# Optimization experiments

Measured on AMD Instinct MI355X. Metric: run time of the kernel, lower is better.

Reference implementation:

```python
import jax, jax.numpy as jnp
import numpy as np

N = 50000       # num vertices
E_SEG = 80000   # num hyperedges
NNZ = 400000    # incidence pairs
FIN = 512       # input feature dim
H = 256         # MLP_hidden
C = 40          # num classes
NLAYER = 2      # All_num_layers
ALPHA = 0.5     # restart_alpha


def _w(k, shape):
    return jax.random.normal(k, shape, jnp.float32) * (1.0 / np.sqrt(shape[0]))


def setup_inputs() -> dict:
    key = jax.random.key(0)
    ks = jax.random.split(key, 12)
    return {
        "x": jax.random.normal(ks[0], (N, FIN), jnp.float32),
        "vertex": jax.random.randint(ks[1], (NNZ,), 0, N),
        "edges": jax.random.randint(ks[2], (NNZ,), 0, E_SEG),
        "lin_in_w": _w(ks[3], (FIN, H)), "lin_in_b": jnp.zeros((H,), jnp.float32),
        "w1": _w(ks[4], (H, H)),   "b1": jnp.zeros((H,), jnp.float32),
        "w2": _w(ks[5], (2 * H, H)), "b2": jnp.zeros((H,), jnp.float32),
        "w3": _w(ks[6], (H, H)),   "b3": jnp.zeros((H,), jnp.float32),
        "cls_w1": _w(ks[7], (H, H)), "cls_b1": jnp.zeros((H,), jnp.float32),
        "cls_w2": _w(ks[8], (H, C)), "cls_b2": jnp.zeros((C,), jnp.float32),
    }


def reference(x, vertex, edges, lin_in_w, lin_in_b, w1, b1, w2, b2, w3, b3,
              cls_w1, cls_b1, cls_w2, cls_b2):
    # input projection (dropout is identity at p=0)
    x = jax.nn.relu(x @ lin_in_w + lin_in_b)           # [N, H]
    x0 = x
    for _ in range(NLAYER):  # same conv weights reused each layer
        # W1 (1-layer MLP = Linear), gather to incidences
        xve = (x @ w1 + b1)[vertex]                    # [NNZ, H]
        # scatter-add to hyperedges
        xe = jax.ops.segment_sum(xve, edges, num_segments=E_SEG)  # [E, H]
        # gather back, concat with vertex feats, W2 (Linear on 2H)
        xev = jnp.concatenate([x[vertex], xe[edges]], axis=-1) @ w2 + b2  # [NNZ, H]
        # scatter-add to vertices
        xv = jax.ops.segment_sum(xev, vertex, num_segments=N)     # [N, H]
        # restart connection + W (Linear) + outer activation
        x = (1.0 - ALPHA) * xv + ALPHA * x0
        x = jax.nn.relu(x @ w3 + b3)
    # classifier MLP (2 layers: Linear -> relu -> Linear)
    h = jax.nn.relu(x @ cls_w1 + cls_b1)
    return h @ cls_w2 + cls_b2                          # [N, C]
```

## Files before the change

### kernel.cpp

```cpp
#include <hip/hip_runtime.h>
#include <hip/hip_bf16.h>
#include <cstdint>
#include <cstddef>

#define HD   256
#define NV   50000
#define NE   80000
#define NNZC 400000
#define FINC 512
#define NCLS 40

using bf16 = __hip_bfloat16;

typedef short bf16x8v __attribute__((ext_vector_type(8)));
typedef float f32x4   __attribute__((ext_vector_type(4)));

#define NCH_E ((NE + 1023) / 1024)
#define NCH_V ((NV + 1023) / 1024)

__device__ __forceinline__ float b2f(unsigned short u) {
    union { unsigned int i; float f; } c; c.i = ((unsigned int)u) << 16; return c.f;
}
__device__ __forceinline__ unsigned short f2b(float f) {
    union { float f; unsigned int i; } c; c.f = f;
    return (unsigned short)((c.i + 0x7FFFu + ((c.i >> 16) & 1u)) >> 16);
}
__device__ __forceinline__ float4 load4f(const bf16* p) {
    ushort4 u = *reinterpret_cast<const ushort4*>(p);
    return make_float4(b2f(u.x), b2f(u.y), b2f(u.z), b2f(u.w));
}
__device__ __forceinline__ void store4(bf16* p, float4 v) {
    ushort4 u; u.x = f2b(v.x); u.y = f2b(v.y); u.z = f2b(v.z); u.w = f2b(v.w);
    *reinterpret_cast<ushort4*>(p) = u;
}

__device__ __forceinline__ void gl_lds16(const bf16* g, short* l) {
    __builtin_amdgcn_global_load_lds(
        (const __attribute__((address_space(1))) unsigned int*)g,
        (__attribute__((address_space(3))) unsigned int*)l,
        16, 0, 0);
}

__global__ __launch_bounds__(256)
void fill0_k(unsigned int* __restrict__ p, long long n)
{
    long long i = (long long)blockIdx.x * 256 + threadIdx.x;
    long long stride = (long long)gridDim.x * 256;
    for (; i < n; i += stride) p[i] = 0u;
}

__global__ __launch_bounds__(256)
void hist_k(const int* __restrict__ vertex, const int* __restrict__ edges,
            int* __restrict__ cnt_v, int* __restrict__ cnt_e, int nnz)
{
    int i = blockIdx.x * 256 + threadIdx.x;
    if (i < nnz) {
        atomicAdd(&cnt_v[vertex[i]], 1);
        atomicAdd(&cnt_e[edges[i]], 1);
    }
}

__global__ __launch_bounds__(256)
void scan_part2_k(const int* __restrict__ cnt_e, int* __restrict__ off_e, int* __restrict__ part_e,
                  const int* __restrict__ cnt_v, int* __restrict__ off_v, int* __restrict__ part_v)
{
    const int* cnt; int* off; int* part; int n;
    if (blockIdx.y == 0) { cnt = cnt_e; off = off_e; part = part_e; n = NE; }
    else                 { cnt = cnt_v; off = off_v; part = part_v; n = NV; }
    int base = blockIdx.x * 1024;
    if (base >= n) return;
    __shared__ int s[256];
    int idx = base + threadIdx.x * 4;
    int v[4], sum = 0;
    #pragma unroll
    for (int j = 0; j < 4; ++j) { v[j] = (idx + j < n) ? cnt[idx + j] : 0; sum += v[j]; }
    s[threadIdx.x] = sum;
    __syncthreads();
    #pragma unroll
    for (int d = 1; d < 256; d <<= 1) {
        int t = (threadIdx.x >= d) ? s[threadIdx.x - d] : 0;
        __syncthreads();
        s[threadIdx.x] += t;
        __syncthreads();
    }
    int excl = s[threadIdx.x] - sum;
    #pragma unroll
    for (int j = 0; j < 4; ++j) {
        if (idx + j < n) off[idx + j] = excl;
        excl += v[j];
    }
    if (threadIdx.x == 255) part[blockIdx.x] = s[255];
}

__global__ __launch_bounds__(256)
void scan_top2_k(int* __restrict__ part_e, int* __restrict__ end_e,
                 int* __restrict__ part_v, int* __restrict__ end_v)
{
    int* part; int* endp; int nch;
    if (blockIdx.x == 0) { part = part_e; endp = end_e; nch = NCH_E; }
    else                 { part = part_v; endp = end_v; nch = NCH_V; }
    __shared__ int s[256];
    int v = (threadIdx.x < nch) ? part[threadIdx.x] : 0;
    s[threadIdx.x] = v;
    __syncthreads();
    #pragma unroll
    for (int d = 1; d < 256; d <<= 1) {
        int t = (threadIdx.x >= d) ? s[threadIdx.x - d] : 0;
        __syncthreads();
        s[threadIdx.x] += t;
        __syncthreads();
    }
    if (threadIdx.x < nch) part[threadIdx.x] = s[threadIdx.x] - v;
    if (threadIdx.x == 255) *endp = s[255];
}

__global__ __launch_bounds__(256)
void scan_addcur2_k(int* __restrict__ off_e, const int* __restrict__ part_e, int* __restrict__ cur_e,
                    int* __restrict__ off_v, const int* __restrict__ part_v, int* __restrict__ cur_v)
{
    int n; int* off; const int* part; int* cur;
    if (blockIdx.y == 0) { n = NE; off = off_e; part = part_e; cur = cur_e; }
    else                 { n = NV; off = off_v; part = part_v; cur = cur_v; }
    int i = blockIdx.x * 256 + threadIdx.x;
    if (i < n) { int o = off[i] + part[i >> 10]; off[i] = o; cur[i] = o; }
}

__global__ __launch_bounds__(256)
void csr_fill_k(const int* __restrict__ vertex, const int* __restrict__ edges,
                int* __restrict__ cur_e, int* __restrict__ cur_v,
                int* __restrict__ adj_e, int* __restrict__ adj_v, int nnz)
{
    int i = blockIdx.x * 256 + threadIdx.x;
    if (i >= nnz) return;
    int v = vertex[i], e = edges[i];
    adj_e[atomicAdd(&cur_e[e], 1)] = v;
    adj_v[atomicAdd(&cur_v[v], 1)] = e;
}

__global__ __launch_bounds__(256)
void prep_w_k(const float* __restrict__ lin_w, const float* __restrict__ w1,
              const float* __restrict__ w2, const float* __restrict__ w3,
              const float* __restrict__ cw1, const float* __restrict__ cw2,
              const float* __restrict__ b2,
              unsigned short* __restrict__ lin_wt, unsigned short* __restrict__ w1t,
              unsigned short* __restrict__ w2a_nb, unsigned short* __restrict__ w2b_nb,
              unsigned short* __restrict__ w3t, unsigned short* __restrict__ cw1t,
              unsigned short* __restrict__ cw2t, float* __restrict__ b2w3)
{
    int idx = blockIdx.x * 256 + threadIdx.x;
    if (idx < 131072) { int n = idx >> 9, k = idx & 511; lin_wt[idx] = f2b(lin_w[k * 256 + n]); return; }
    idx -= 131072;
    if (idx < 65536) { int n = idx >> 8, k = idx & 255; w1t[idx] = f2b(w1[k * 256 + n]); return; }
    idx -= 65536;
    if (idx < 65536) { w2a_nb[idx] = f2b(w2[idx]); return; }
    idx -= 65536;
    if (idx < 65536) { w2b_nb[idx] = f2b(w2[65536 + idx]); return; }
    idx -= 65536;
    if (idx < 65536) { int n = idx >> 8, k = idx & 255; w3t[idx] = f2b(w3[k * 256 + n]); return; }
    idx -= 65536;
    if (idx < 65536) { int n = idx >> 8, k = idx & 255; cw1t[idx] = f2b(cw1[k * 256 + n]); return; }
    idx -= 65536;
    if (idx < 12288) { int n = idx >> 8, k = idx & 255; cw2t[idx] = f2b((n < NCLS) ? cw2[k * NCLS + n] : 0.f); return; }
    idx -= 12288;
    if (idx < 256) {
        float s = 0.f;
        for (int k = 0; k < 256; ++k) s += b2[k] * w3[k * 256 + idx];
        b2w3[idx] = s;
    }
}

template<int EPI, bool AF32>
__global__ __launch_bounds__(256)
void mgemm_k(const void* __restrict__ Agv, const bf16* __restrict__ Bt,
             const float* __restrict__ bias, const float* __restrict__ bias2,
             const int* __restrict__ deg,
             const bf16* __restrict__ Sb, const bf16* __restrict__ z0b,
             const float* __restrict__ b2w3v,
             bf16* __restrict__ Cg, bf16* __restrict__ Cg2, bf16* __restrict__ Cg3,
             int M, int K, int Nc)
{
    const int nbn = Nc >> 7;
    const int nbm = (M + 127) >> 7;
    const int p   = blockIdx.x;
    const int xcd = p & 7;
    const int q   = p >> 3;
    const int cblk = q % nbn;
    const int rblk = q / nbn;
    const int rb   = rblk * 8 + xcd;
    if (rb >= nbm) return;
    const int bn = cblk * 128;
    const int bm = rb * 128;

    __shared__ __align__(16) short As[128 * 64];
    __shared__ __align__(16) short Bs[128 * 64];

    const int t  = threadIdx.x;
    const int wv = t >> 6, l = t & 63;
    const int wr = wv >> 1, wc = wv & 1;
    const int l15 = l & 15;

    f32x4 acc[4][4];
    #pragma unroll
    for (int m = 0; m < 4; ++m)
        #pragma unroll
        for (int n = 0; n < 4; ++n)
            acc[m][n] = (f32x4){0.f, 0.f, 0.f, 0.f};

    const int brow8   = l >> 3;
    const int bcol_sw = (((l & 7) ^ (l >> 3)) * 8);

    for (int k0 = 0; k0 < K; k0 += 64) {
        if constexpr (AF32) {
            const float* Af = (const float*)Agv;
            #pragma unroll
            for (int pi = 0; pi < 4; ++pi) {
                int idx8 = pi * 256 + t;
                int row  = idx8 >> 3;
                int cg   = (idx8 & 7) * 8;
                int ga = bm + row; if (ga >= M) ga = M - 1;
                const float* src = Af + (size_t)ga * K + k0 + cg;
                f32x4 u = *reinterpret_cast<const f32x4*>(src);
                f32x4 v = *reinterpret_cast<const f32x4*>(src + 4);
                bf16x8v o;
                o[0] = (short)f2b(u[0]); o[1] = (short)f2b(u[1]);
                o[2] = (short)f2b(u[2]); o[3] = (short)f2b(u[3]);
                o[4] = (short)f2b(v[0]); o[5] = (short)f2b(v[1]);
                o[6] = (short)f2b(v[2]); o[7] = (short)f2b(v[3]);
                *reinterpret_cast<bf16x8v*>(As + row * 64 + (cg ^ ((row & 7) * 8))) = o;
            }
        } else {
            const bf16* Ab = (const bf16*)Agv;
            #pragma unroll
            for (int i = 0; i < 4; ++i) {
                int c = wv * 4 + i;
                int row = c * 8 + brow8;
                int ga = bm + row; if (ga >= M) ga = M - 1;
                gl_lds16(Ab + (size_t)ga * K + k0 + bcol_sw, As + c * 512);
            }
        }
        #pragma unroll
        for (int i = 0; i < 4; ++i) {
            int c = wv * 4 + i;
            int row = c * 8 + brow8;
            gl_lds16(Bt + (size_t)(bn + row) * K + k0 + bcol_sw, Bs + c * 512);
        }
        __syncthreads();

        #pragma unroll
        for (int ks = 0; ks < 2; ++ks) {
            bf16x8v a[4], b[4];
            const int kb = ks * 64 + (l >> 4) * 16;
            #pragma unroll
            for (int m = 0; m < 4; ++m) {
                int r = wr * 64 + m * 16 + l15;
                a[m] = *reinterpret_cast<const bf16x8v*>(
                           (const char*)As + r * 128 + (kb ^ ((r & 7) << 4)));
            }
            #pragma unroll
            for (int n = 0; n < 4; ++n) {
                int r = wc * 64 + n * 16 + l15;
                b[n] = *reinterpret_cast<const bf16x8v*>(
                           (const char*)Bs + r * 128 + (kb ^ ((r & 7) << 4)));
            }
            #pragma unroll
            for (int m = 0; m < 4; ++m)
                #pragma unroll
                for (int n = 0; n < 4; ++n)
                    acc[m][n] = __builtin_amdgcn_mfma_f32_16x16x32_bf16(a[m], b[n], acc[m][n], 0, 0, 0);
        }
        __syncthreads();
    }

    if (EPI == 3) {
        int oi = bn >> 8;
        bf16* CC = (oi == 0) ? Cg : (oi == 1) ? Cg2 : Cg3;
        const float* bb = (oi == 0) ? bias : (oi == 1) ? bias2 : nullptr;
        int cb = bn & 255;
        float bv[4];
        #pragma unroll
        for (int n = 0; n < 4; ++n)
            bv[n] = bb ? bb[cb + wc * 64 + n * 16 + l15] : 0.f;
        #pragma unroll
        for (int m = 0; m < 4; ++m) {
            #pragma unroll
            for (int i = 0; i < 4; ++i) {
                int row = bm + wr * 64 + m * 16 + (l >> 4) * 4 + i;
                if (row >= M) continue;
                size_t base = (size_t)row * 256 + cb + wc * 64 + l15;
                #pragma unroll
                for (int n = 0; n < 4; ++n)
                    reinterpret_cast<unsigned short*>(CC)[base + n * 16] = f2b(acc[m][n][i] + bv[n]);
            }
        }
    } else if (EPI == 4) {
        float bv[4], bw[4];
        #pragma unroll
        for (int n = 0; n < 4; ++n) {
            int col = bn + wc * 64 + n * 16 + l15;
            bv[n] = bias[col];
            bw[n] = b2w3v[col];
        }
        #pragma unroll
        for (int m = 0; m < 4; ++m) {
            #pragma unroll
            for (int i = 0; i < 4; ++i) {
                int row = bm + wr * 64 + m * 16 + (l >> 4) * 4 + i;
                if (row >= M) continue;
                float d = (float)deg[row];
                size_t base = (size_t)row * Nc + bn + wc * 64 + l15;
                #pragma unroll
                for (int n = 0; n < 4; ++n) {
                    size_t idx = base + (size_t)n * 16;
                    float sv = b2f(reinterpret_cast<const unsigned short*>(Sb)[idx]);
                    float zv = b2f(reinterpret_cast<const unsigned short*>(z0b)[idx]);
                    float v = 0.5f * (d * (sv + bw[n]) + acc[m][n][i]) + 0.5f * zv + bv[n];
                    v = fmaxf(v, 0.f);
                    reinterpret_cast<unsigned short*>(Cg)[idx] = f2b(v);
                }
            }
        }
    } else {
        float bv[4];
        #pragma unroll
        for (int n = 0; n < 4; ++n)
            bv[n] = bias ? bias[bn + wc * 64 + n * 16 + l15] : 0.f;
        #pragma unroll
        for (int m = 0; m < 4; ++m) {
            #pragma unroll
            for (int i = 0; i < 4; ++i) {
                int row = bm + wr * 64 + m * 16 + (l >> 4) * 4 + i;
                if (row >= M) continue;
                size_t base = (size_t)row * Nc + bn + wc * 64 + l15;
                #pragma unroll
                for (int n = 0; n < 4; ++n) {
                    float v = acc[m][n][i] + bv[n];
                    if (EPI == 1) v = fmaxf(v, 0.f);
                    reinterpret_cast<unsigned short*>(Cg)[base + n * 16] = f2b(v);
                }
            }
        }
    }
}

__global__ __launch_bounds__(256)
void gather_sum_k(const bf16* __restrict__ src, const int* __restrict__ adj,
                  const int* __restrict__ off, bf16* __restrict__ dst, int nseg)
{
    int seg = blockIdx.x * 4 + (threadIdx.x >> 6);
    if (seg >= nseg) return;
    int lane = threadIdx.x & 63;
    int s0 = off[seg], s1 = off[seg + 1];
    float4 acc = make_float4(0.f, 0.f, 0.f, 0.f);
    int j = s0;
    for (; j + 4 <= s1; j += 4) {
        int r0 = adj[j], r1 = adj[j + 1], r2 = adj[j + 2], r3 = adj[j + 3];
        float4 v0 = load4f(src + (size_t)r0 * HD + lane * 4);
        float4 v1 = load4f(src + (size_t)r1 * HD + lane * 4);
        float4 v2 = load4f(src + (size_t)r2 * HD + lane * 4);
        float4 v3 = load4f(src + (size_t)r3 * HD + lane * 4);
        acc.x += (v0.x + v1.x) + (v2.x + v3.x);
        acc.y += (v0.y + v1.y) + (v2.y + v3.y);
        acc.z += (v0.z + v1.z) + (v2.z + v3.z);
        acc.w += (v0.w + v1.w) + (v2.w + v3.w);
    }
    for (; j < s1; ++j) {
        float4 v = load4f(src + (size_t)adj[j] * HD + lane * 4);
        acc.x += v.x; acc.y += v.y; acc.z += v.z; acc.w += v.w;
    }
    store4(dst + (size_t)seg * HD + lane * 4, acc);
}

__global__ __launch_bounds__(256)
void cls_mfma_k(const bf16* __restrict__ Hm, const bf16* __restrict__ Wt,
                const float* __restrict__ bias, float* __restrict__ out, int M)
{
    const int wv = threadIdx.x >> 6, l = threadIdx.x & 63;
    const int l15 = l & 15;
    const int r0 = blockIdx.x * 64 + wv * 16;
    f32x4 acc[3];
    #pragma unroll
    for (int n = 0; n < 3; ++n) acc[n] = (f32x4){0.f, 0.f, 0.f, 0.f};

    int arow = r0 + l15; if (arow >= M) arow = M - 1;
    const int ko = (l >> 4) * 8;
    for (int kk = 0; kk < HD; kk += 32) {
        bf16x8v a = *reinterpret_cast<const bf16x8v*>(Hm + (size_t)arow * HD + kk + ko);
        #pragma unroll
        for (int n = 0; n < 3; ++n) {
            bf16x8v b = *reinterpret_cast<const bf16x8v*>(Wt + (size_t)(n * 16 + l15) * HD + kk + ko);
            acc[n] = __builtin_amdgcn_mfma_f32_16x16x32_bf16(a, b, acc[n], 0, 0, 0);
        }
    }
    #pragma unroll
    for (int n = 0; n < 3; ++n) {
        int col = n * 16 + l15;
        if (col >= NCLS) continue;
        float bv = bias[col];
        #pragma unroll
        for (int i = 0; i < 4; ++i) {
            int row = r0 + (l >> 4) * 4 + i;
            if (row < M) out[(size_t)row * NCLS + col] = acc[n][i] + bv;
        }
    }
}

static inline int xcd_grid(int M, int Nc)
{
    int nbm = (M + 127) >> 7;
    int nbn = Nc >> 7;
    return nbn * (((nbm + 7) / 8) * 8);
}

extern "C" void kernel_launch(void* const* d_in, const int* in_sizes, int n_in,
                              void* d_out, int out_size, void* d_ws, size_t ws_size,
                              hipStream_t stream)
{
    const float* x_in   = (const float*)d_in[0];
    const int*   vertex = (const int*)d_in[1];
    const int*   edges  = (const int*)d_in[2];
    const float* lin_w  = (const float*)d_in[3];
    const float* lin_b  = (const float*)d_in[4];
    const float* w1     = (const float*)d_in[5];
    const float* b1     = (const float*)d_in[6];
    const float* w2     = (const float*)d_in[7];
    const float* b2     = (const float*)d_in[8];
    const float* w3     = (const float*)d_in[9];
    const float* b3     = (const float*)d_in[10];
    const float* cw1    = (const float*)d_in[11];
    const float* cb1    = (const float*)d_in[12];
    const float* cw2    = (const float*)d_in[13];
    const float* cb2    = (const float*)d_in[14];
    float* out = (float*)d_out;
    (void)in_sizes; (void)n_in; (void)out_size; (void)ws_size;

    char* ws = (char*)d_ws;
    const size_t nvhd = (size_t)NV * HD, nehd = (size_t)NE * HD;
    size_t off = 0;
    auto alloc = [&](size_t bytes) { char* p = ws + off; off += (bytes + 255) & ~(size_t)255; return p; };
    bf16* x0 = (bf16*)alloc(nvhd * 2);
    bf16* xA = (bf16*)alloc(nvhd * 2);
    bf16* E1 = (bf16*)alloc(nehd * 2);
    bf16* E2 = (bf16*)alloc(nehd * 2);
    bf16* S  = (bf16*)alloc(nvhd * 2);
    bf16* z0 = (bf16*)alloc(nvhd * 2);
    unsigned short* w1t    = (unsigned short*)alloc(3 * 256 * 256 * 2);
    unsigned short* W23at  = w1t + 65536;
    unsigned short* w3t    = w1t + 131072;
    unsigned short* W23bt  = (unsigned short*)alloc(256 * 256 * 2);
    unsigned short* w2ab   = (unsigned short*)alloc(512 * 256 * 2);
    unsigned short* w2a_nb = w2ab;
    unsigned short* w2b_nb = w2ab + 256 * 256;
    unsigned short* lin_wt = (unsigned short*)alloc(256 * 512 * 2);
    unsigned short* cw1t   = (unsigned short*)alloc(256 * 256 * 2);
    unsigned short* cw2t   = (unsigned short*)alloc(48 * 256 * 2);
    float* b2w3 = (float*)alloc(256 * 4);
    int* cnt_e = (int*)alloc(NE * 4);
    int* cnt_v = (int*)alloc(NV * 4);
    int* off_e = (int*)alloc((NE + 1) * 4);
    int* off_v = (int*)alloc((NV + 1) * 4);
    int* cur_e = (int*)alloc(NE * 4);
    int* cur_v = (int*)alloc(NV * 4);
    int* part_e = (int*)alloc(256 * 4);
    int* part_v = (int*)alloc(256 * 4);
    int* adj_e = (int*)alloc((size_t)NNZC * 4);
    int* adj_v = (int*)alloc((size_t)NNZC * 4);

    dim3 blk(256);

    fill0_k<<<128, blk, 0, stream>>>((unsigned int*)cnt_e, NE + NV);
    hist_k<<<(NNZC + 255) / 256, blk, 0, stream>>>(vertex, edges, cnt_v, cnt_e, NNZC);
    scan_part2_k<<<dim3(NCH_E, 2), blk, 0, stream>>>(cnt_e, off_e, part_e, cnt_v, off_v, part_v);
    scan_top2_k<<<2, blk, 0, stream>>>(part_e, off_e + NE, part_v, off_v + NV);
    scan_addcur2_k<<<dim3((NE + 255) / 256, 2), blk, 0, stream>>>(off_e, part_e, cur_e,
                                                                  off_v, part_v, cur_v);
    csr_fill_k<<<(NNZC + 255) / 256, blk, 0, stream>>>(vertex, edges, cur_e, cur_v, adj_e, adj_v, NNZC);

    prep_w_k<<<1841, blk, 0, stream>>>(lin_w, w1, w2, w3, cw1, cw2, b2,
                                       lin_wt, w1t, w2a_nb, w2b_nb, w3t, cw1t, cw2t, b2w3);
    mgemm_k<3, false><<<xcd_grid(256, 512), blk, 0, stream>>>((const bf16*)w3t, (const bf16*)w2ab,
        nullptr, nullptr, nullptr, nullptr, nullptr, nullptr,
        (bf16*)W23at, (bf16*)W23bt, nullptr, 256, 256, 512);

    mgemm_k<1, true><<<xcd_grid(NV, 256), blk, 0, stream>>>(x_in, (const bf16*)lin_wt,
        lin_b, nullptr, nullptr, nullptr, nullptr, nullptr,
        x0, nullptr, nullptr, NV, FINC, HD);

    const bf16* cur = x0;
    for (int layer = 0; layer < 2; ++layer) {
        if (layer == 0) {
            mgemm_k<3, false><<<xcd_grid(NV, 768), blk, 0, stream>>>(cur, (const bf16*)w1t,
                b1, nullptr, nullptr, nullptr, nullptr, nullptr,
                E1, S, z0, NV, HD, 768);
        } else {
            mgemm_k<3, false><<<xcd_grid(NV, 512), blk, 0, stream>>>(cur, (const bf16*)w1t,
                b1, nullptr, nullptr, nullptr, nullptr, nullptr,
                E1, S, nullptr, NV, HD, 512);
        }
        gather_sum_k<<<(NE + 3) / 4, blk, 0, stream>>>(E1, adj_e, off_e, E2, NE);
        gather_sum_k<<<(NV + 3) / 4, blk, 0, stream>>>(E2, adj_v, off_v, E1, NV);
        mgemm_k<4, false><<<xcd_grid(NV, 256), blk, 0, stream>>>(E1, (const bf16*)W23bt,
            b3, nullptr, cnt_v, S, z0, b2w3,
            xA, nullptr, nullptr, NV, HD, HD);
        cur = xA;
    }

    mgemm_k<1, false><<<xcd_grid(NV, 256), blk, 0, stream>>>(xA, (const bf16*)cw1t,
        cb1, nullptr, nullptr, nullptr, nullptr, nullptr,
        E1, nullptr, nullptr, NV, HD, HD);
    cls_mfma_k<<<(NV + 63) / 64, blk, 0, stream>>>(E1, (const bf16*)cw2t, cb2, out, NV);
}
```

Baseline: 470.8 us.

## Fuse vertex gather-sum into the W23 GEMM epilogue kernel

```diff
diff --git a/kernel.cpp b/kernel.cpp
--- a/kernel.cpp
+++ b/kernel.cpp
@@ -337,6 +337,134 @@
                     if (EPI == 1) v = fmaxf(v, 0.f);
                     reinterpret_cast<unsigned short*>(Cg)[base + n * 16] = f2b(v);
                 }
+            }
+        }
+    }
+}
+
+__global__ __launch_bounds__(256)
+void epi4g_k(const bf16* __restrict__ xe, const int* __restrict__ adj,
+             const int* __restrict__ off, const bf16* __restrict__ Bt,
+             const float* __restrict__ b3v, const float* __restrict__ b2w3v,
+             const int* __restrict__ deg,
+             const bf16* __restrict__ Sb, const bf16* __restrict__ z0b,
+             bf16* __restrict__ Cg, int M)
+{
+    __shared__ __align__(16) short As[64 * 256];
+    __shared__ __align__(16) short Bs[256 * 64];
+
+    const int t  = threadIdx.x;
+    const int wv = t >> 6, l = t & 63;
+    const int l15 = l & 15;
+    const int bm = blockIdx.x * 64;
+
+    const int brow8   = l >> 3;
+    const int bcol_sw = (((l & 7) ^ (l >> 3)) * 8);
+
+    #pragma unroll
+    for (int i = 0; i < 8; ++i) {
+        int c = wv * 8 + i;
+        int row = c * 8 + brow8;
+        gl_lds16(Bt + (size_t)row * 256 + bcol_sw, Bs + c * 512);
+    }
+
+    for (int rr = 0; rr < 16; ++rr) {
+        int r = wv * 16 + rr;
+        int v = bm + r;
+        float4 acc = make_float4(0.f, 0.f, 0.f, 0.f);
+        if (v < M) {
+            int s0 = off[v], s1 = off[v + 1];
+            int j = s0;
+            for (; j + 4 <= s1; j += 4) {
+                int r0 = adj[j], r1 = adj[j + 1], r2 = adj[j + 2], r3 = adj[j + 3];
+                float4 v0 = load4f(xe + (size_t)r0 * HD + l * 4);
+                float4 v1 = load4f(xe + (size_t)r1 * HD + l * 4);
+                float4 v2 = load4f(xe + (size_t)r2 * HD + l * 4);
+                float4 v3 = load4f(xe + (size_t)r3 * HD + l * 4);
+                acc.x += (v0.x + v1.x) + (v2.x + v3.x);
+                acc.y += (v0.y + v1.y) + (v2.y + v3.y);
+                acc.z += (v0.z + v1.z) + (v2.z + v3.z);
+                acc.w += (v0.w + v1.w) + (v2.w + v3.w);
+            }
+            for (; j < s1; ++j) {
+                float4 vv = load4f(xe + (size_t)adj[j] * HD + l * 4);
+                acc.x += vv.x; acc.y += vv.y; acc.z += vv.z; acc.w += vv.w;
+            }
+        }
+        short4 o;
+        o.x = (short)f2b(acc.x); o.y = (short)f2b(acc.y);
+        o.z = (short)f2b(acc.z); o.w = (short)f2b(acc.w);
+        int cb = l * 8;
+        *reinterpret_cast<short4*>((char*)As + r * 512 + (cb ^ ((r & 7) << 4))) = o;
+    }
+    __syncthreads();
+
+    f32x4 acc[4][4];
+    #pragma unroll
+    for (int m = 0; m < 4; ++m)
+        #pragma unroll
+        for (int n = 0; n < 4; ++n)
+            acc[m][n] = (f32x4){0.f, 0.f, 0.f, 0.f};
+
+    #pragma unroll
+    for (int k0 = 0; k0 < 4; ++k0) {
+        #pragma unroll
+        for (int ks = 0; ks < 2; ++ks) {
+            bf16x8v a[4], b[4];
+            const int kb = ks * 64 + (l >> 4) * 16;
+            #pragma unroll
+            for (int m = 0; m < 4; ++m) {
+                int r = m * 16 + l15;
+                a[m] = *reinterpret_cast<const bf16x8v*>(
+                           (const char*)As + r * 512 + ((k0 * 128 + kb) ^ ((r & 7) << 4)));
+            }
+            #pragma unroll
+            for (int n = 0; n < 4; ++n) {
+                int r = wv * 64 + n * 16 + l15;
+                b[n] = *reinterpret_cast<const bf16x8v*>(
+                           (const char*)Bs + r * 128 + (kb ^ ((r & 7) << 4)));
+            }
+            #pragma unroll
+            for (int m = 0; m < 4; ++m)
+                #pragma unroll
+                for (int n = 0; n < 4; ++n)
+                    acc[m][n] = __builtin_amdgcn_mfma_f32_16x16x32_bf16(a[m], b[n], acc[m][n], 0, 0, 0);
+        }
+        __syncthreads();
+        if (k0 < 3) {
+            #pragma unroll
+            for (int i = 0; i < 8; ++i) {
+                int c = wv * 8 + i;
+                int row = c * 8 + brow8;
+                gl_lds16(Bt + (size_t)row * 256 + (k0 + 1) * 64 + bcol_sw, Bs + c * 512);
+            }
+            __syncthreads();
+        }
+    }
+
+    float bv[4], bw[4];
+    #pragma unroll
+    for (int n = 0; n < 4; ++n) {
+        int col = wv * 64 + n * 16 + l15;
+        bv[n] = b3v[col];
+        bw[n] = b2w3v[col];
+    }
+    #pragma unroll
+    for (int m = 0; m < 4; ++m) {
+        #pragma unroll
+        for (int i = 0; i < 4; ++i) {
+            int row = bm + m * 16 + (l >> 4) * 4 + i;
+            if (row >= M) continue;
+            float d = (float)deg[row];
+            size_t base = (size_t)row * 256 + wv * 64 + l15;
+            #pragma unroll
+            for (int n = 0; n < 4; ++n) {
+                size_t idx = base + (size_t)n * 16;
+                float sv = b2f(reinterpret_cast<const unsigned short*>(Sb)[idx]);
+                float zv = b2f(reinterpret_cast<const unsigned short*>(z0b)[idx]);
+                float v = 0.5f * (d * (sv + bw[n]) + acc[m][n][i]) + 0.5f * zv + bv[n];
+                v = fmaxf(v, 0.f);
+                reinterpret_cast<unsigned short*>(Cg)[idx] = f2b(v);
             }
         }
     }
@@ -497,10 +625,8 @@
                 E1, S, nullptr, NV, HD, 512);
         }
         gather_sum_k<<<(NE + 3) / 4, blk, 0, stream>>>(E1, adj_e, off_e, E2, NE);
-        gather_sum_k<<<(NV + 3) / 4, blk, 0, stream>>>(E2, adj_v, off_v, E1, NV);
-        mgemm_k<4, false><<<xcd_grid(NV, 256), blk, 0, stream>>>(E1, (const bf16*)W23bt,
-            b3, nullptr, cnt_v, S, z0, b2w3,
-            xA, nullptr, nullptr, NV, HD, HD);
+        epi4g_k<<<(NV + 63) / 64, blk, 0, stream>>>(E2, adj_v, off_v, (const bf16*)W23bt,
+            b3, b2w3, cnt_v, S, z0, xA, NV);
         cur = xA;
     }
 
```

New measurement: 549.8 us. 1.17x slower.

## Fold W1 into the post-aggregation weight and gather raw vertex features

Applied to the files above, without the earlier changes.

```diff
diff --git a/kernel.cpp b/kernel.cpp
--- a/kernel.cpp
+++ b/kernel.cpp
@@ -138,11 +138,32 @@
 }
 
 __global__ __launch_bounds__(256)
+void dege2_k(const int* __restrict__ cnt_e, const int* __restrict__ adj_v,
+             const int* __restrict__ off_v, int* __restrict__ dege2, int n)
+{
+    int v = blockIdx.x * 256 + threadIdx.x;
+    if (v >= n) return;
+    int s = 0;
+    for (int j = off_v[v]; j < off_v[v + 1]; ++j) s += cnt_e[adj_v[j]];
+    dege2[v] = s;
+}
+
+__global__ __launch_bounds__(256)
+void b1w23_k(const float* __restrict__ b1, const unsigned short* __restrict__ W23bt,
+             float* __restrict__ o)
+{
+    int n = threadIdx.x;
+    float s = 0.f;
+    for (int k = 0; k < 256; ++k) s += b1[k] * b2f(W23bt[n * 256 + k]);
+    o[n] = s;
+}
+
+__global__ __launch_bounds__(256)
 void prep_w_k(const float* __restrict__ lin_w, const float* __restrict__ w1,
               const float* __restrict__ w2, const float* __restrict__ w3,
               const float* __restrict__ cw1, const float* __restrict__ cw2,
               const float* __restrict__ b2,
-              unsigned short* __restrict__ lin_wt, unsigned short* __restrict__ w1t,
+              unsigned short* __restrict__ lin_wt, unsigned short* __restrict__ w1_nb,
               unsigned short* __restrict__ w2a_nb, unsigned short* __restrict__ w2b_nb,
               unsigned short* __restrict__ w3t, unsigned short* __restrict__ cw1t,
               unsigned short* __restrict__ cw2t, float* __restrict__ b2w3)
@@ -150,7 +171,7 @@
     int idx = blockIdx.x * 256 + threadIdx.x;
     if (idx < 131072) { int n = idx >> 9, k = idx & 511; lin_wt[idx] = f2b(lin_w[k * 256 + n]); return; }
     idx -= 131072;
-    if (idx < 65536) { int n = idx >> 8, k = idx & 255; w1t[idx] = f2b(w1[k * 256 + n]); return; }
+    if (idx < 65536) { w1_nb[idx] = f2b(w1[idx]); return; }
     idx -= 65536;
     if (idx < 65536) { w2a_nb[idx] = f2b(w2[idx]); return; }
     idx -= 65536;
@@ -173,9 +194,9 @@
 __global__ __launch_bounds__(256)
 void mgemm_k(const void* __restrict__ Agv, const bf16* __restrict__ Bt,
              const float* __restrict__ bias, const float* __restrict__ bias2,
-             const int* __restrict__ deg,
+             const int* __restrict__ deg, const int* __restrict__ dege2,
              const bf16* __restrict__ Sb, const bf16* __restrict__ z0b,
-             const float* __restrict__ b2w3v,
+             const float* __restrict__ b2w3v, const float* __restrict__ b1w23v,
              bf16* __restrict__ Cg, bf16* __restrict__ Cg2, bf16* __restrict__ Cg3,
              int M, int K, int Nc)
 {
@@ -293,12 +314,13 @@
             }
         }
     } else if (EPI == 4) {
-        float bv[4], bw[4];
+        float bv[4], bw[4], bb1[4];
         #pragma unroll
         for (int n = 0; n < 4; ++n) {
             int col = bn + wc * 64 + n * 16 + l15;
-            bv[n] = bias[col];
-            bw[n] = b2w3v[col];
+            bv[n]  = bias[col];
+            bw[n]  = b2w3v[col];
+            bb1[n] = b1w23v[col];
         }
         #pragma unroll
         for (int m = 0; m < 4; ++m) {
@@ -306,14 +328,16 @@
             for (int i = 0; i < 4; ++i) {
                 int row = bm + wr * 64 + m * 16 + (l >> 4) * 4 + i;
                 if (row >= M) continue;
-                float d = (float)deg[row];
+                float d   = (float)deg[row];
+                float de2 = (float)dege2[row];
                 size_t base = (size_t)row * Nc + bn + wc * 64 + l15;
                 #pragma unroll
                 for (int n = 0; n < 4; ++n) {
                     size_t idx = base + (size_t)n * 16;
                     float sv = b2f(reinterpret_cast<const unsigned short*>(Sb)[idx]);
                     float zv = b2f(reinterpret_cast<const unsigned short*>(z0b)[idx]);
-                    float v = 0.5f * (d * (sv + bw[n]) + acc[m][n][i]) + 0.5f * zv + bv[n];
+                    float v = 0.5f * (d * (sv + bw[n]) + acc[m][n][i] + de2 * bb1[n])
+                              + 0.5f * zv + bv[n];
                     v = fmaxf(v, 0.f);
                     reinterpret_cast<unsigned short*>(Cg)[idx] = f2b(v);
                 }
@@ -443,19 +467,22 @@
     bf16* E2 = (bf16*)alloc(nehd * 2);
     bf16* S  = (bf16*)alloc(nvhd * 2);
     bf16* z0 = (bf16*)alloc(nvhd * 2);
-    unsigned short* w1t    = (unsigned short*)alloc(3 * 256 * 256 * 2);
-    unsigned short* W23at  = w1t + 65536;
-    unsigned short* w3t    = w1t + 131072;
+    unsigned short* W23at  = (unsigned short*)alloc(2 * 256 * 256 * 2);
+    unsigned short* w3t    = W23at + 65536;
     unsigned short* W23bt  = (unsigned short*)alloc(256 * 256 * 2);
+    unsigned short* W123bt = (unsigned short*)alloc(256 * 256 * 2);
     unsigned short* w2ab   = (unsigned short*)alloc(512 * 256 * 2);
     unsigned short* w2a_nb = w2ab;
     unsigned short* w2b_nb = w2ab + 256 * 256;
+    unsigned short* w1_nb  = (unsigned short*)alloc(256 * 256 * 2);
     unsigned short* lin_wt = (unsigned short*)alloc(256 * 512 * 2);
     unsigned short* cw1t   = (unsigned short*)alloc(256 * 256 * 2);
     unsigned short* cw2t   = (unsigned short*)alloc(48 * 256 * 2);
-    float* b2w3 = (float*)alloc(256 * 4);
+    float* b2w3  = (float*)alloc(256 * 4);
+    float* b1w23 = (float*)alloc(256 * 4);
     int* cnt_e = (int*)alloc(NE * 4);
     int* cnt_v = (int*)alloc(NV * 4);
+    int* dege2 = (int*)alloc(NV * 4);
     int* off_e = (int*)alloc((NE + 1) * 4);
     int* off_v = (int*)alloc((NV + 1) * 4);
     int* cur_e = (int*)alloc(NE * 4);
@@ -474,38 +501,43 @@
     scan_addcur2_k<<<dim3((NE + 255) / 256, 2), blk, 0, stream>>>(off_e, part_e, cur_e,
                                                                   off_v, part_v, cur_v);
     csr_fill_k<<<(NNZC + 255) / 256, blk, 0, stream>>>(vertex, edges, cur_e, cur_v, adj_e, adj_v, NNZC);
+    dege2_k<<<(NV + 255) / 256, blk, 0, stream>>>(cnt_e, adj_v, off_v, dege2, NV);
 
     prep_w_k<<<1841, blk, 0, stream>>>(lin_w, w1, w2, w3, cw1, cw2, b2,
-                                       lin_wt, w1t, w2a_nb, w2b_nb, w3t, cw1t, cw2t, b2w3);
+                                       lin_wt, w1_nb, w2a_nb, w2b_nb, w3t, cw1t, cw2t, b2w3);
     mgemm_k<3, false><<<xcd_grid(256, 512), blk, 0, stream>>>((const bf16*)w3t, (const bf16*)w2ab,
-        nullptr, nullptr, nullptr, nullptr, nullptr, nullptr,
+        nullptr, nullptr, nullptr, nullptr, nullptr, nullptr, nullptr, nullptr,
         (bf16*)W23at, (bf16*)W23bt, nullptr, 256, 256, 512);
+    mgemm_k<0, false><<<xcd_grid(256, 256), blk, 0, stream>>>((const bf16*)W23bt, (const bf16*)w1_nb,
+        nullptr, nullptr, nullptr, nullptr, nullptr, nullptr, nullptr, nullptr,
+        (bf16*)W123bt, nullptr, nullptr, 256, 256, 256);
+    b1w23_k<<<1, blk, 0, stream>>>(b1, W23bt, b1w23);
 
     mgemm_k<1, true><<<xcd_grid(NV, 256), blk, 0, stream>>>(x_in, (const bf16*)lin_wt,
-        lin_b, nullptr, nullptr, nullptr, nullptr, nullptr,
+        lin_b, nullptr, nullptr, nullptr, nullptr, nullptr, nullptr, nullptr,
         x0, nullptr, nullptr, NV, FINC, HD);
 
     const bf16* cur = x0;
     for (int layer = 0; layer < 2; ++layer) {
         if (layer == 0) {
-            mgemm_k<3, false><<<xcd_grid(NV, 768), blk, 0, stream>>>(cur, (const bf16*)w1t,
-                b1, nullptr, nullptr, nullptr, nullptr, nullptr,
-                E1, S, z0, NV, HD, 768);
+            mgemm_k<3, false><<<xcd_grid(NV, 512), blk, 0, stream>>>(cur, (const bf16*)W23at,
+                nullptr, nullptr, nullptr, nullptr, nullptr, nullptr, nullptr, nullptr,
+                S, z0, nullptr, NV, HD, 512);
         } else {
-            mgemm_k<3, false><<<xcd_grid(NV, 512), blk, 0, stream>>>(cur, (const bf16*)w1t,
-                b1, nullptr, nullptr, nullptr, nullptr, nullptr,
-                E1, S, nullptr, NV, HD, 512);
-        }
-        gather_sum_k<<<(NE + 3) / 4, blk, 0, stream>>>(E1, adj_e, off_e, E2, NE);
+            mgemm_k<0, false><<<xcd_grid(NV, 256), blk, 0, stream>>>(cur, (const bf16*)W23at,
+                nullptr, nullptr, nullptr, nullptr, nullptr, nullptr, nullptr, nullptr,
+                S, nullptr, nullptr, NV, HD, HD);
+        }
+        gather_sum_k<<<(NE + 3) / 4, blk, 0, stream>>>(cur, adj_e, off_e, E2, NE);
         gather_sum_k<<<(NV + 3) / 4, blk, 0, stream>>>(E2, adj_v, off_v, E1, NV);
-        mgemm_k<4, false><<<xcd_grid(NV, 256), blk, 0, stream>>>(E1, (const bf16*)W23bt,
-            b3, nullptr, cnt_v, S, z0, b2w3,
+        mgemm_k<4, false><<<xcd_grid(NV, 256), blk, 0, stream>>>(E1, (const bf16*)W123bt,
+            b3, nullptr, cnt_v, dege2, S, z0, b2w3, b1w23,
             xA, nullptr, nullptr, NV, HD, HD);
         cur = xA;
     }
 
     mgemm_k<1, false><<<xcd_grid(NV, 256), blk, 0, stream>>>(xA, (const bf16*)cw1t,
-        cb1, nullptr, nullptr, nullptr, nullptr, nullptr,
+        cb1, nullptr, nullptr, nullptr, nullptr, nullptr, nullptr, nullptr,
         E1, nullptr, nullptr, NV, HD, HD);
     cls_mfma_k<<<(NV + 63) / 64, blk, 0, stream>>>(E1, (const bf16*)cw2t, cb2, out, NV);
 }
```

Result: no change. 474.5 us (+0.8%).
